# Optimization experiments

Hardware: AMD Instinct MI355X
Metric: run time of the kernel (lower is better)

The kernel has to match this reference:

```python
import jax, jax.numpy as jnp
import numpy as np

N_NODES = 10000
N_EDGES = 160000
F_IN = 2613
D = 256
H = 4
NEG_SLOPE = 0.2
BN_EPS = 1e-5


def _bn(h, g, b):
    # BatchNorm1d in training mode: batch statistics, biased variance
    return (h - h.mean(0)) / jnp.sqrt(h.var(0) + BN_EPS) * g + b


def _gat_conv(h_in, src, dst, n, W, att_src, att_dst, bias):
    # PyG GATConv, concat=True: h_in [n, F] -> [n, H*D]
    h = (h_in @ W).reshape(n, H, D)                      # [n, H, D]
    a_src = jnp.sum(h * att_src, axis=-1)                # [n, H]
    a_dst = jnp.sum(h * att_dst, axis=-1)                # [n, H]
    e = jax.nn.leaky_relu(a_src[src] + a_dst[dst], NEG_SLOPE)  # [E, H]
    # segment softmax over destination nodes (stable)
    m = jax.ops.segment_max(e, dst, num_segments=n)
    e = jnp.exp(e - m[dst])
    denom = jax.ops.segment_sum(e, dst, num_segments=n)
    alpha = e / (denom[dst] + 1e-16)                     # [E, H]
    out = jax.ops.segment_sum(h[src] * alpha[:, :, None], dst, num_segments=n)
    return out.reshape(n, H * D) + bias


def setup_inputs() -> dict:
    key = jax.random.key(0)
    ks = jax.random.split(key, 24)
    s = 0.02
    inp = {
        "x": jax.random.normal(ks[0], (N_NODES, F_IN), jnp.float32),
        "edges": jax.random.randint(ks[1], (2, N_EDGES), 0, N_NODES, jnp.int64),
        # MLP stack
        "W1": jax.random.normal(ks[2], (F_IN, D), jnp.float32) * s,
        "b1": jnp.zeros((D,), jnp.float32),
        "W2": jax.random.normal(ks[3], (D, D), jnp.float32) * s,
        "b2": jnp.zeros((D,), jnp.float32),
        "W3": jax.random.normal(ks[4], (D, D), jnp.float32) * s,
        "b3": jnp.zeros((D,), jnp.float32),
        # BatchNorm affine params
        "g1": jnp.ones((D,), jnp.float32), "be1": jnp.zeros((D,), jnp.float32),
        "g2": jnp.ones((D,), jnp.float32), "be2": jnp.zeros((D,), jnp.float32),
        "g3": jnp.ones((D,), jnp.float32), "be3": jnp.zeros((D,), jnp.float32),
        "g4": jnp.ones((H * D,), jnp.float32), "be4": jnp.zeros((H * D,), jnp.float32),
        "Wg1": jax.random.normal(ks[5], (D, H * D), jnp.float32) * s,
        "as1": jax.random.normal(ks[6], (H, D), jnp.float32) * s,
        "ad1": jax.random.normal(ks[7], (H, D), jnp.float32) * s,
        "bg1": jnp.zeros((H * D,), jnp.float32),
        "Wg2": jax.random.normal(ks[8], (H * D, H * D), jnp.float32) * s,
        "as2": jax.random.normal(ks[9], (H, D), jnp.float32) * s,
        "ad2": jax.random.normal(ks[10], (H, D), jnp.float32) * s,
        "bg2": jnp.zeros((H * D,), jnp.float32),
    }
    return inp


def reference(x, edges, W1, b1, W2, b2, W3, b3,
              g1, be1, g2, be2, g3, be3, g4, be4,
              Wg1, as1, ad1, bg1, Wg2, as2, ad2, bg2):
    n = x.shape[0]
    src, dst = edges[0], edges[1]
    # PyG: remove existing self-loops then add one per node. We reroute
    # accidental self-loops deterministically, then append self-loops.
    dst = jnp.where(src == dst, (dst + 1) % n, dst)
    loops = jnp.arange(n, dtype=src.dtype)
    src = jnp.concatenate([src, loops])
    dst = jnp.concatenate([dst, loops])

    h = jax.nn.elu(_bn(x @ W1 + b1, g1, be1))
    h = jax.nn.elu(_bn(h @ W2 + b2, g2, be2))
    h = jax.nn.elu(_bn(h @ W3 + b3, g3, be3))
    h = _gat_conv(h, src, dst, n, Wg1, as1, ad1, bg1)
    h = jax.nn.elu(_bn(h, g4, be4))
    h = _gat_conv(h, src, dst, n, Wg2, as2, ad2, bg2)
    return h
```

## Files before the change

### kernel.cpp

```cpp
#include <hip/hip_runtime.h>
#include <hip/hip_bf16.h>

typedef __attribute__((ext_vector_type(8))) short short8v;
typedef __attribute__((ext_vector_type(4))) float f32x4;

__device__ inline float b2f(ushort u) {
  union { uint i; float f; } c;
  c.i = (uint)u << 16;
  return c.f;
}
__device__ inline ushort f2b(float f) {
  __hip_bfloat16 h = __float2bfloat16(f);
  return *(ushort*)&h;
}

typedef __attribute__((address_space(1))) const unsigned int guint;
typedef __attribute__((address_space(3))) unsigned int luint;
__device__ __forceinline__ void gload16(const void* g, void* l) {
  __builtin_amdgcn_global_load_lds((guint*)g, (luint*)l, 16, 0, 0);
}

template <bool BN, bool ALIGNED>
__global__ __launch_bounds__(256) void gemm_bn(
    const float* __restrict__ A, const __hip_bfloat16* __restrict__ Bh,
    const __hip_bfloat16* __restrict__ Bl, const float* __restrict__ sc,
    const float* __restrict__ sh, float* __restrict__ P, int M, int N, int K,
    int Kp, int nc, int nr, int nz) {
  __shared__ ushort Ash[128][40];
  __shared__ ushort Asl[128][40];
  __shared__ ushort Bs2[2][128][32];
  __shared__ ushort Bl2[2][128][32];
  const int nwg = gridDim.x;
  const int b = blockIdx.x;
  const int l = (b & 7) * (nwg >> 3) + (b >> 3);
  const int cb = l % nc;
  const int rr = (l / nc) % nr;
  const int z = l / (nc * nr);

  const int tid = threadIdx.x;
  const int lane = tid & 63;
  const int w = tid >> 6, wr = w >> 1, wc = w & 1;
  const int brow = rr * 128, bcol = cb * 128;
  const int l15 = lane & 15, koff = (lane >> 4) * 8;
  const int arow = tid >> 1, aseg = (tid & 1) * 16;
  const int srow = tid >> 2, sseg = (tid & 3) * 8;
  const int nK = (K + 31) >> 5;
  const int ks0 = (nK * z) / nz, ks1 = (nK * (z + 1)) / nz;

  f32x4 acc[4][4] = {};

  const int ar = brow + arow;
  const bool arv = ar < M;
  const float* Arow = A + (long)ar * K;
  const ushort* gBh0 = (const ushort*)Bh + (long)(bcol + srow) * Kp + sseg;
  const ushort* gBh1 = (const ushort*)Bh + (long)(bcol + 64 + srow) * Kp + sseg;
  const ushort* gBl0 = (const ushort*)Bl + (long)(bcol + srow) * Kp + sseg;
  const ushort* gBl1 = (const ushort*)Bl + (long)(bcol + 64 + srow) * Kp + sseg;
  const int lo0 = (w * 64) << 3;
  const int lo1 = (256 + w * 64) << 3;

  float av[16];
  auto loadAv = [&](int ks) {
    const int kb = (ks << 5) + aseg;
    if (arv) {
      if (ALIGNED) {
        const float4* ap = (const float4*)(Arow + kb);
#pragma unroll
        for (int q = 0; q < 4; ++q) {
          float4 f = ap[q];
          av[q * 4 + 0] = f.x;
          av[q * 4 + 1] = f.y;
          av[q * 4 + 2] = f.z;
          av[q * 4 + 3] = f.w;
        }
      } else {
        if (kb + 16 <= K) {
#pragma unroll
          for (int j = 0; j < 16; ++j) av[j] = Arow[kb + j];
        } else {
#pragma unroll
          for (int j = 0; j < 16; ++j) av[j] = (kb + j < K) ? Arow[kb + j] : 0.f;
        }
      }
    } else {
#pragma unroll
      for (int j = 0; j < 16; ++j) av[j] = 0.f;
    }
  };

  if (ks0 < ks1) {
    loadAv(ks0);
    const int k0 = ks0 << 5;
    gload16(gBh0 + k0, &Bs2[0][0][0] + lo0);
    gload16(gBh1 + k0, &Bs2[0][0][0] + lo1);
    gload16(gBl0 + k0, &Bl2[0][0][0] + lo0);
    gload16(gBl1 + k0, &Bl2[0][0][0] + lo1);
  }

  for (int ks = ks0; ks < ks1; ++ks) {
    const int cur = (ks - ks0) & 1;
    const int kbase = (ks << 5) + aseg;
    if (BN && arv) {
#pragma unroll
      for (int q = 0; q < 4; ++q) {
        float4 c4 = *(const float4*)(sc + kbase + q * 4);
        float4 h4 = *(const float4*)(sh + kbase + q * 4);
        float* a4 = &av[q * 4];
        a4[0] = fmaf(a4[0], c4.x, h4.x);
        a4[1] = fmaf(a4[1], c4.y, h4.y);
        a4[2] = fmaf(a4[2], c4.z, h4.z);
        a4[3] = fmaf(a4[3], c4.w, h4.w);
      }
#pragma unroll
      for (int j = 0; j < 16; ++j) {
        float v = av[j];
        av[j] = v > 0.f ? v : (__expf(v) - 1.f);
      }
    }
    short8v ah0, ah1, al0, al1;
#pragma unroll
    for (int j = 0; j < 8; ++j) {
      {
        uint u = __float_as_uint(av[j]);
        ah0[j] = (short)(u >> 16);
        al0[j] = (short)f2b(av[j] - __uint_as_float(u & 0xFFFF0000u));
      }
      {
        uint u = __float_as_uint(av[j + 8]);
        ah1[j] = (short)(u >> 16);
        al1[j] = (short)f2b(av[j + 8] - __uint_as_float(u & 0xFFFF0000u));
      }
    }
    __syncthreads();
    *(short8v*)&Ash[arow][aseg] = ah0;
    *(short8v*)&Ash[arow][aseg + 8] = ah1;
    *(short8v*)&Asl[arow][aseg] = al0;
    *(short8v*)&Asl[arow][aseg + 8] = al1;
    __syncthreads();
    if (ks + 1 < ks1) {
      const int k0n = (ks + 1) << 5;
      const int nxt = cur ^ 1;
      ushort* bh = &Bs2[nxt][0][0];
      ushort* bl = &Bl2[nxt][0][0];
      gload16(gBh0 + k0n, bh + lo0);
      gload16(gBh1 + k0n, bh + lo1);
      gload16(gBl0 + k0n, bl + lo0);
      gload16(gBl1 + k0n, bl + lo1);
      loadAv(ks + 1);
    }
    short8v bfh[4], bfl[4];
#pragma unroll
    for (int nn = 0; nn < 4; ++nn) {
      bfh[nn] = *(const short8v*)&Bs2[cur][wc * 64 + nn * 16 + l15][koff];
      bfl[nn] = *(const short8v*)&Bl2[cur][wc * 64 + nn * 16 + l15][koff];
    }
#pragma unroll
    for (int m = 0; m < 4; ++m) {
      short8v afh = *(const short8v*)&Ash[wr * 64 + m * 16 + l15][koff];
      short8v afl = *(const short8v*)&Asl[wr * 64 + m * 16 + l15][koff];
#pragma unroll
      for (int nn = 0; nn < 4; ++nn) {
        acc[m][nn] = __builtin_amdgcn_mfma_f32_16x16x32_bf16(afh, bfh[nn], acc[m][nn], 0, 0, 0);
        acc[m][nn] = __builtin_amdgcn_mfma_f32_16x16x32_bf16(afh, bfl[nn], acc[m][nn], 0, 0, 0);
        acc[m][nn] = __builtin_amdgcn_mfma_f32_16x16x32_bf16(afl, bfh[nn], acc[m][nn], 0, 0, 0);
      }
    }
  }

  float* outp = P + (long)z * M * N;
#pragma unroll
  for (int m = 0; m < 4; ++m) {
#pragma unroll
    for (int nn = 0; nn < 4; ++nn) {
      int col = bcol + wc * 64 + nn * 16 + l15;
#pragma unroll
      for (int r = 0; r < 4; ++r) {
        int row = brow + wr * 64 + m * 16 + (lane >> 4) * 4 + r;
        if (row < M) outp[(long)row * N + col] = acc[m][nn][r];
      }
    }
  }
}

__global__ __launch_bounds__(256) void gemm_bf16(
    const ushort* __restrict__ A, const __hip_bfloat16* __restrict__ B,
    ushort* __restrict__ C, int M, int N, int K, int nc, int nr) {
  __shared__ ushort A2[2][128][32];
  __shared__ ushort B2[2][128][32];
  const int nwg = gridDim.x;
  const int b = blockIdx.x;
  const int l = (b & 7) * (nwg >> 3) + (b >> 3);
  const int cb = l % nc;
  const int rr = l / nc;

  const int tid = threadIdx.x;
  const int lane = tid & 63;
  const int w = tid >> 6, wr = w >> 1, wc = w & 1;
  const int brow = rr * 128, bcol = cb * 128;
  const int l15 = lane & 15, koff = (lane >> 4) * 8;
  const int srow = tid >> 2, sseg = (tid & 3) * 8;
  const int nK = K >> 5;

  f32x4 acc[4][4] = {};

  const ushort* gA0 = A + (long)(brow + srow) * K + sseg;
  const ushort* gA1 = A + (long)(brow + 64 + srow) * K + sseg;
  const ushort* gB0 = (const ushort*)B + (long)(bcol + srow) * K + sseg;
  const ushort* gB1 = (const ushort*)B + (long)(bcol + 64 + srow) * K + sseg;
  const int lo0 = (w * 64) << 3;
  const int lo1 = (256 + w * 64) << 3;

  gload16(gA0, &A2[0][0][0] + lo0);
  gload16(gA1, &A2[0][0][0] + lo1);
  gload16(gB0, &B2[0][0][0] + lo0);
  gload16(gB1, &B2[0][0][0] + lo1);

  for (int ks = 0; ks < nK; ++ks) {
    const int cur = ks & 1;
    __syncthreads();
    if (ks + 1 < nK) {
      const int k0n = (ks + 1) << 5;
      const int nxt = cur ^ 1;
      gload16(gA0 + k0n, &A2[nxt][0][0] + lo0);
      gload16(gA1 + k0n, &A2[nxt][0][0] + lo1);
      gload16(gB0 + k0n, &B2[nxt][0][0] + lo0);
      gload16(gB1 + k0n, &B2[nxt][0][0] + lo1);
    }
    short8v bf[4];
#pragma unroll
    for (int nn = 0; nn < 4; ++nn)
      bf[nn] = *(const short8v*)&B2[cur][wc * 64 + nn * 16 + l15][koff];
#pragma unroll
    for (int m = 0; m < 4; ++m) {
      short8v af = *(const short8v*)&A2[cur][wr * 64 + m * 16 + l15][koff];
#pragma unroll
      for (int nn = 0; nn < 4; ++nn)
        acc[m][nn] = __builtin_amdgcn_mfma_f32_16x16x32_bf16(af, bf[nn], acc[m][nn], 0, 0, 0);
    }
  }

#pragma unroll
  for (int m = 0; m < 4; ++m) {
#pragma unroll
    for (int nn = 0; nn < 4; ++nn) {
      int col = bcol + wc * 64 + nn * 16 + l15;
#pragma unroll
      for (int r = 0; r < 4; ++r) {
        int row = brow + wr * 64 + m * 16 + (lane >> 4) * 4 + r;
        if (row < M) C[(long)row * N + col] = f2b(acc[m][nn][r]);
      }
    }
  }
}

__global__ __launch_bounds__(256) void bn_elu_b16(
    const float* __restrict__ h, const float* __restrict__ sc,
    const float* __restrict__ sh, ushort* __restrict__ o, long MN, int N) {
  long nq = MN >> 2;
  for (long q = blockIdx.x * 256LL + threadIdx.x; q < nq;
       q += (long)gridDim.x * 256LL) {
    long i = q << 2;
    int col = (int)(i % N);
    float4 v = *(const float4*)(h + i);
    float4 c = *(const float4*)(sc + col);
    float4 s = *(const float4*)(sh + col);
    float a0 = fmaf(v.x, c.x, s.x);
    float a1 = fmaf(v.y, c.y, s.y);
    float a2 = fmaf(v.z, c.z, s.z);
    float a3 = fmaf(v.w, c.w, s.w);
    a0 = a0 > 0.f ? a0 : (__expf(a0) - 1.f);
    a1 = a1 > 0.f ? a1 : (__expf(a1) - 1.f);
    a2 = a2 > 0.f ? a2 : (__expf(a2) - 1.f);
    a3 = a3 > 0.f ? a3 : (__expf(a3) - 1.f);
    ushort4 r;
    r.x = f2b(a0);
    r.y = f2b(a1);
    r.z = f2b(a2);
    r.w = f2b(a3);
    *(ushort4*)(o + i) = r;
  }
}

template <bool BIAS, bool STATS>
__global__ __launch_bounds__(256) void reduce_post(
    const float* __restrict__ P, const float* __restrict__ bias,
    float* __restrict__ C, float* __restrict__ osum, float* __restrict__ osq,
    long MN, int N, int Z) {
  const int col = (int)((blockIdx.x * 256 + threadIdx.x) % N);
  const float bv = BIAS ? bias[col] : 0.f;
  float ps = 0.f, pq = 0.f;
  for (long i = blockIdx.x * 256LL + threadIdx.x; i < MN;
       i += (long)gridDim.x * 256LL) {
    float s = bv;
    for (int zz = 0; zz < Z; ++zz) s += P[(long)zz * MN + i];
    C[i] = s;
    if (STATS) {
      ps += s;
      pq += s * s;
    }
  }
  if (STATS) {
    atomicAdd(&osum[col], ps);
    atomicAdd(&osq[col], pq);
  }
}

__global__ __launch_bounds__(256) void bn_coef(
    const float* __restrict__ ssum, const float* __restrict__ ssq,
    const float* __restrict__ g, const float* __restrict__ be,
    float* __restrict__ sc, float* __restrict__ sh, int N, float invM) {
  int c = blockIdx.x * 256 + threadIdx.x;
  if (c >= N) return;
  float mean = ssum[c] * invM;
  float var = ssq[c] * invM - mean * mean;
  float s = rsqrtf(var + 1e-5f) * g[c];
  sc[c] = s;
  sh[c] = be[c] - mean * s;
}

template <bool LO>
__global__ __launch_bounds__(256) void trans_split(
    const float* __restrict__ W, __hip_bfloat16* __restrict__ Oh,
    __hip_bfloat16* __restrict__ Ol, int K, int N, int Kp) {
  __shared__ float tile[64][65];
  const int k0 = blockIdx.x * 64, n0 = blockIdx.y * 64;
  const int tx = threadIdx.x & 63, ty = threadIdx.x >> 6;
#pragma unroll
  for (int j = 0; j < 16; ++j) {
    int r = ty * 16 + j;
    int k = k0 + r;
    tile[r][tx] = (k < K) ? W[(long)k * N + n0 + tx] : 0.f;
  }
  __syncthreads();
#pragma unroll
  for (int j = 0; j < 16; ++j) {
    int a = ty * 16 + j;
    float v = tile[tx][a];
    long o = (long)(n0 + a) * Kp + k0 + tx;
    if (LO) {
      uint u = __float_as_uint(v);
      ushort hu = (ushort)(u >> 16);
      Oh[o] = *(__hip_bfloat16*)&hu;
      ushort lu = f2b(v - __uint_as_float(u & 0xFFFF0000u));
      Ol[o] = *(__hip_bfloat16*)&lu;
    } else {
      ushort hu = f2b(v);
      Oh[o] = *(__hip_bfloat16*)&hu;
    }
  }
}

__global__ __launch_bounds__(256) void bn_stats(
    const float* __restrict__ h, int M, int N, float* __restrict__ sum,
    float* __restrict__ sumsq) {
  int col = blockIdx.y * 256 + threadIdx.x;
  float s = 0.f, sq = 0.f;
  for (int r = blockIdx.x; r < M; r += gridDim.x) {
    float v = h[(long)r * N + col];
    s += v;
    sq += v * v;
  }
  atomicAdd(&sum[col], s);
  atomicAdd(&sumsq[col], sq);
}

__global__ __launch_bounds__(256) void att_scores_bf16(
    const ushort* __restrict__ hgb, const float* __restrict__ att_s,
    const float* __restrict__ att_d, float* __restrict__ a_src,
    float* __restrict__ a_dst, int n) {
  int node = blockIdx.x;
  int h = threadIdx.x >> 6, lane = threadIdx.x & 63;
  int c = lane * 4;
  ushort4 hv = *(const ushort4*)(hgb + (long)node * 1024 + h * 256 + c);
  float4 as = *(const float4*)(att_s + h * 256 + c);
  float4 ad = *(const float4*)(att_d + h * 256 + c);
  float x0 = b2f(hv.x), x1 = b2f(hv.y), x2 = b2f(hv.z), x3 = b2f(hv.w);
  float ss = x0 * as.x + x1 * as.y + x2 * as.z + x3 * as.w;
  float sd = x0 * ad.x + x1 * ad.y + x2 * ad.z + x3 * ad.w;
#pragma unroll
  for (int off = 32; off; off >>= 1) {
    ss += __shfl_down(ss, off);
    sd += __shfl_down(sd, off);
  }
  if (lane == 0) {
    a_src[node * 4 + h] = ss;
    a_dst[node * 4 + h] = sd;
  }
}

__global__ __launch_bounds__(256) void deg_count(
    const int* __restrict__ srcA, const int* __restrict__ dstA,
    int* __restrict__ deg, int n, int E0, int E) {
  int e = blockIdx.x * blockDim.x + threadIdx.x;
  if (e >= E) return;
  int d;
  if (e < E0) {
    int s = srcA[e];
    d = dstA[e];
    if (s == d) d = (d + 1) % n;
  } else {
    d = e - E0;
  }
  atomicAdd(&deg[d], 1);
}

__global__ __launch_bounds__(256) void scan_rows(
    const int* __restrict__ deg, int* __restrict__ row_start, int n) {
  __shared__ int sums[256];
  int t = threadIdx.x;
  int chunk = (n + 255) / 256;
  int start = t * chunk, end = min(start + chunk, n);
  int s = 0;
  for (int i = start; i < end; ++i) s += deg[i];
  sums[t] = s;
  __syncthreads();
  for (int off = 1; off < 256; off <<= 1) {
    int v = (t >= off) ? sums[t - off] : 0;
    __syncthreads();
    sums[t] += v;
    __syncthreads();
  }
  int run = (t == 0) ? 0 : sums[t - 1];
  for (int i = start; i < end; ++i) {
    row_start[i] = run;
    run += deg[i];
  }
  if (t == 255) row_start[n] = run;
}

__global__ __launch_bounds__(256) void scatter_edges(
    const int* __restrict__ srcA, const int* __restrict__ dstA,
    int* __restrict__ cursor, int* __restrict__ csr_src, int n, int E0, int E) {
  int e = blockIdx.x * blockDim.x + threadIdx.x;
  if (e >= E) return;
  int s, d;
  if (e < E0) {
    s = srcA[e];
    d = dstA[e];
    if (s == d) d = (d + 1) % n;
  } else {
    s = d = e - E0;
  }
  int pos = atomicAdd(&cursor[d], 1);
  csr_src[pos] = s;
}

__global__ __launch_bounds__(256) void aggregate_fused(
    const ushort* __restrict__ hgb, const int* __restrict__ row_start,
    const int* __restrict__ csr_src, const float* __restrict__ a_src,
    const float* __restrict__ a_dst, const float* __restrict__ bias,
    float* __restrict__ out) {
  int d = blockIdx.x;
  int t = threadIdx.x;
  int hh = t >> 6;
  int off = hh * 256 + (t & 63) * 4;
  int p0 = row_start[d], p1 = row_start[d + 1];
  float adv = a_dst[d * 4 + hh];
  float den = 1e-16f;
  float4 acc = {0.f, 0.f, 0.f, 0.f};
  for (int p = p0; p < p1; ++p) {
    int s = csr_src[p];
    float v = a_src[s * 4 + hh] + adv;
    v = v > 0.f ? v : 0.2f * v;
    float ex = __expf(v);
    den += ex;
    ushort4 hv = *(const ushort4*)(hgb + (long)s * 1024 + off);
    acc.x += ex * b2f(hv.x);
    acc.y += ex * b2f(hv.y);
    acc.z += ex * b2f(hv.z);
    acc.w += ex * b2f(hv.w);
  }
  float rden = 1.f / den;
  float4 bv = *(const float4*)(bias + off);
  float4 o;
  o.x = bv.x + acc.x * rden;
  o.y = bv.y + acc.y * rden;
  o.z = bv.z + acc.z * rden;
  o.w = bv.w + acc.w * rden;
  *(float4*)(out + (long)d * 1024 + off) = o;
}

extern "C" void kernel_launch(void* const* d_in, const int* in_sizes, int n_in,
                              void* d_out, int out_size, void* d_ws,
                              size_t ws_size, hipStream_t stream) {
  const float* x = (const float*)d_in[0];
  const int* edges = (const int*)d_in[1];
  const float* W1 = (const float*)d_in[2];
  const float* b1 = (const float*)d_in[3];
  const float* W2 = (const float*)d_in[4];
  const float* b2 = (const float*)d_in[5];
  const float* W3 = (const float*)d_in[6];
  const float* b3 = (const float*)d_in[7];
  const float* g1 = (const float*)d_in[8];
  const float* be1 = (const float*)d_in[9];
  const float* g2 = (const float*)d_in[10];
  const float* be2 = (const float*)d_in[11];
  const float* g3 = (const float*)d_in[12];
  const float* be3 = (const float*)d_in[13];
  const float* g4 = (const float*)d_in[14];
  const float* be4 = (const float*)d_in[15];
  const float* Wg1 = (const float*)d_in[16];
  const float* as1 = (const float*)d_in[17];
  const float* ad1 = (const float*)d_in[18];
  const float* bg1 = (const float*)d_in[19];
  const float* Wg2 = (const float*)d_in[20];
  const float* as2 = (const float*)d_in[21];
  const float* ad2 = (const float*)d_in[22];
  const float* bg2 = (const float*)d_in[23];
  float* out = (float*)d_out;

  const int n = 10000, E0 = 160000, E = 170000;
  const int F = 2613, Fp = 2624, D = 256, HD = 1024;
  const int* srcA = edges;
  const int* dstA = edges + E0;

  uint8_t* p = (uint8_t*)d_ws;
  auto alloc = [&](size_t bytes) -> void* {
    void* r = (void*)p;
    p += (bytes + 255) & ~(size_t)255;
    return r;
  };
  float* h1 = (float*)alloc((size_t)n * D * 4);
  float* h2 = (float*)alloc((size_t)n * D * 4);
  float* h3 = (float*)alloc((size_t)n * D * 4);
  float* agg = (float*)alloc((size_t)n * HD * 4);
  float* pbuf = (float*)alloc((size_t)8 * n * D * 4);
  ushort* hgb = (ushort*)alloc((size_t)n * HD * 2);
  ushort* actb = (ushort*)alloc((size_t)n * HD * 2);
  __hip_bfloat16* W1h = (__hip_bfloat16*)alloc((size_t)D * Fp * 2);
  __hip_bfloat16* W1l = (__hip_bfloat16*)alloc((size_t)D * Fp * 2);
  __hip_bfloat16* W2h = (__hip_bfloat16*)alloc((size_t)D * D * 2);
  __hip_bfloat16* W2l = (__hip_bfloat16*)alloc((size_t)D * D * 2);
  __hip_bfloat16* W3h = (__hip_bfloat16*)alloc((size_t)D * D * 2);
  __hip_bfloat16* W3l = (__hip_bfloat16*)alloc((size_t)D * D * 2);
  __hip_bfloat16* Wg1h = (__hip_bfloat16*)alloc((size_t)HD * D * 2);
  __hip_bfloat16* Wg2h = (__hip_bfloat16*)alloc((size_t)HD * HD * 2);
  float* asrc = (float*)alloc((size_t)n * 4 * 4);
  float* adst = (float*)alloc((size_t)n * 4 * 4);
  float* sc1 = (float*)alloc(D * 4);
  float* sh1 = (float*)alloc(D * 4);
  float* sc2 = (float*)alloc(D * 4);
  float* sh2 = (float*)alloc(D * 4);
  float* sc3 = (float*)alloc(D * 4);
  float* sh3 = (float*)alloc(D * 4);
  float* sc4 = (float*)alloc(HD * 4);
  float* sh4 = (float*)alloc(HD * 4);
  int* row_start = (int*)alloc((size_t)(n + 1) * 4);
  int* cursor = (int*)alloc((size_t)n * 4);
  int* csr_src = (int*)alloc((size_t)E * 4);
  uint8_t* z0 = p;
  float* ssum1 = (float*)alloc(D * 4);
  float* ssq1 = (float*)alloc(D * 4);
  float* ssum2 = (float*)alloc(D * 4);
  float* ssq2 = (float*)alloc(D * 4);
  float* ssum3 = (float*)alloc(D * 4);
  float* ssq3 = (float*)alloc(D * 4);
  float* ssum4 = (float*)alloc(HD * 4);
  float* ssq4 = (float*)alloc(HD * 4);
  int* deg = (int*)alloc((size_t)n * 4);
  size_t zbytes = (size_t)(p - z0);

  dim3 blk(256);
  const int rb = (n + 127) / 128;
  const int eb = (E + 255) / 256;
  const long MN_D = (long)n * D;
  const long MN_HD = (long)n * HD;
  const float invM = 1.f / (float)n;
  const int gL1 = 2 * rb * 8;
  const int gMLP = 2 * rb * 4;
  const int gGAT = 8 * rb;

  hipMemsetAsync(z0, 0, zbytes, stream);

  deg_count<<<eb, blk, 0, stream>>>(srcA, dstA, deg, n, E0, E);
  scan_rows<<<1, blk, 0, stream>>>(deg, row_start, n);
  hipMemcpyAsync(cursor, row_start, n * sizeof(int), hipMemcpyDeviceToDevice, stream);
  scatter_edges<<<eb, blk, 0, stream>>>(srcA, dstA, cursor, csr_src, n, E0, E);

  trans_split<true><<<dim3(Fp / 64, D / 64), blk, 0, stream>>>(W1, W1h, W1l, F, D, Fp);
  trans_split<true><<<dim3(D / 64, D / 64), blk, 0, stream>>>(W2, W2h, W2l, D, D, D);
  trans_split<true><<<dim3(D / 64, D / 64), blk, 0, stream>>>(W3, W3h, W3l, D, D, D);
  trans_split<false><<<dim3(D / 64, HD / 64), blk, 0, stream>>>(Wg1, Wg1h, nullptr, D, HD, D);
  trans_split<false><<<dim3(HD / 64, HD / 64), blk, 0, stream>>>(Wg2, Wg2h, nullptr, HD, HD, HD);

  gemm_bn<false, false><<<gL1, blk, 0, stream>>>(
      x, W1h, W1l, nullptr, nullptr, pbuf, n, D, F, Fp, 2, rb, 8);
  reduce_post<true, true><<<512, blk, 0, stream>>>(pbuf, b1, h1, ssum1, ssq1, MN_D, D, 8);
  bn_coef<<<1, blk, 0, stream>>>(ssum1, ssq1, g1, be1, sc1, sh1, D, invM);

  gemm_bn<true, true><<<gMLP, blk, 0, stream>>>(
      h1, W2h, W2l, sc1, sh1, pbuf, n, D, D, D, 2, rb, 4);
  reduce_post<true, true><<<512, blk, 0, stream>>>(pbuf, b2, h2, ssum2, ssq2, MN_D, D, 4);
  bn_coef<<<1, blk, 0, stream>>>(ssum2, ssq2, g2, be2, sc2, sh2, D, invM);

  gemm_bn<true, true><<<gMLP, blk, 0, stream>>>(
      h2, W3h, W3l, sc2, sh2, pbuf, n, D, D, D, 2, rb, 4);
  reduce_post<true, true><<<512, blk, 0, stream>>>(pbuf, b3, h3, ssum3, ssq3, MN_D, D, 4);
  bn_coef<<<1, blk, 0, stream>>>(ssum3, ssq3, g3, be3, sc3, sh3, D, invM);

  bn_elu_b16<<<1024, blk, 0, stream>>>(h3, sc3, sh3, actb, MN_D, D);
  gemm_bf16<<<gGAT, blk, 0, stream>>>(actb, Wg1h, hgb, n, HD, D, 8, rb);
  att_scores_bf16<<<n, blk, 0, stream>>>(hgb, as1, ad1, asrc, adst, n);
  aggregate_fused<<<n, blk, 0, stream>>>(hgb, row_start, csr_src, asrc, adst, bg1, agg);

  bn_stats<<<dim3(64, HD / 256), blk, 0, stream>>>(agg, n, HD, ssum4, ssq4);
  bn_coef<<<4, blk, 0, stream>>>(ssum4, ssq4, g4, be4, sc4, sh4, HD, invM);
  bn_elu_b16<<<2048, blk, 0, stream>>>(agg, sc4, sh4, actb, MN_HD, HD);

  gemm_bf16<<<gGAT, blk, 0, stream>>>(actb, Wg2h, hgb, n, HD, HD, 8, rb);
  att_scores_bf16<<<n, blk, 0, stream>>>(hgb, as2, ad2, asrc, adst, n);
  aggregate_fused<<<n, blk, 0, stream>>>(hgb, row_start, csr_src, asrc, adst, bg2, out);
}
```

Measured before the change: 560.9 us.

## Convert input to bf16 and use single-precision-bf16 GEMM for first layer

Adds a pre-pass that converts the fp32 input features to zero-padded bf16. The first MLP GEMM then runs through a generalized bf16 GEMM kernel with split-K instead of the three-MFMA hi/lo split emulation. W1 keeps only its high part, and the split-K factor drops from 8 to 4, shrinking the partial buffer. This removes two thirds of the matrix-core work on the largest GEMM, at the cost of an extra conversion pass over the input and reduced numerical accuracy.

```diff
diff --git a/kernel.cpp b/kernel.cpp
--- a/kernel.cpp
+++ b/kernel.cpp
@@ -20,7 +20,105 @@
   __builtin_amdgcn_global_load_lds((guint*)g, (luint*)l, 16, 0, 0);
 }
 
-template <bool BN, bool ALIGNED>
+__global__ __launch_bounds__(256) void cvt_pad(
+    const float* __restrict__ x, ushort* __restrict__ xb, int K, int Kp) {
+  __shared__ ushort row[2624];
+  const int r = blockIdx.x;
+  const float* src = x + (long)r * K;
+  for (int c = threadIdx.x; c < Kp; c += 256)
+    row[c] = (c < K) ? f2b(src[c]) : (ushort)0;
+  __syncthreads();
+  ushort* dst = xb + (long)r * Kp;
+  const int nchunk = Kp >> 3;
+  for (int c = threadIdx.x; c < nchunk; c += 256)
+    *(short8v*)(dst + c * 8) = *(const short8v*)(row + c * 8);
+}
+
+template <bool B16O>
+__global__ __launch_bounds__(256) void gemm_bf16(
+    const ushort* __restrict__ A, const __hip_bfloat16* __restrict__ B,
+    ushort* __restrict__ Cb, float* __restrict__ P, int M, int N, int K,
+    int nc, int nr, int nz) {
+  __shared__ ushort A2[2][128][32];
+  __shared__ ushort B2[2][128][32];
+  const int nwg = gridDim.x;
+  const int b = blockIdx.x;
+  const int l = (b & 7) * (nwg >> 3) + (b >> 3);
+  const int cb = l % nc;
+  const int rr = (l / nc) % nr;
+  const int z = l / (nc * nr);
+
+  const int tid = threadIdx.x;
+  const int lane = tid & 63;
+  const int w = tid >> 6, wr = w >> 1, wc = w & 1;
+  const int brow = rr * 128, bcol = cb * 128;
+  const int l15 = lane & 15, koff = (lane >> 4) * 8;
+  const int srow = tid >> 2, sseg = (tid & 3) * 8;
+  const int nK = K >> 5;
+  const int ks0 = (nK * z) / nz, ks1 = (nK * (z + 1)) / nz;
+
+  f32x4 acc[4][4] = {};
+
+  const ushort* gA0 = A + (long)(brow + srow) * K + sseg;
+  const ushort* gA1 = A + (long)(brow + 64 + srow) * K + sseg;
+  const ushort* gB0 = (const ushort*)B + (long)(bcol + srow) * K + sseg;
+  const ushort* gB1 = (const ushort*)B + (long)(bcol + 64 + srow) * K + sseg;
+  const int lo0 = (w * 64) << 3;
+  const int lo1 = (256 + w * 64) << 3;
+
+  if (ks0 < ks1) {
+    const int k0 = ks0 << 5;
+    gload16(gA0 + k0, &A2[0][0][0] + lo0);
+    gload16(gA1 + k0, &A2[0][0][0] + lo1);
+    gload16(gB0 + k0, &B2[0][0][0] + lo0);
+    gload16(gB1 + k0, &B2[0][0][0] + lo1);
+  }
+
+  for (int ks = ks0; ks < ks1; ++ks) {
+    const int cur = (ks - ks0) & 1;
+    __syncthreads();
+    if (ks + 1 < ks1) {
+      const int k0n = (ks + 1) << 5;
+      const int nxt = cur ^ 1;
+      gload16(gA0 + k0n, &A2[nxt][0][0] + lo0);
+      gload16(gA1 + k0n, &A2[nxt][0][0] + lo1);
+      gload16(gB0 + k0n, &B2[nxt][0][0] + lo0);
+      gload16(gB1 + k0n, &B2[nxt][0][0] + lo1);
+    }
+    short8v bf[4];
+#pragma unroll
+    for (int nn = 0; nn < 4; ++nn)
+      bf[nn] = *(const short8v*)&B2[cur][wc * 64 + nn * 16 + l15][koff];
+#pragma unroll
+    for (int m = 0; m < 4; ++m) {
+      short8v af = *(const short8v*)&A2[cur][wr * 64 + m * 16 + l15][koff];
+#pragma unroll
+      for (int nn = 0; nn < 4; ++nn)
+        acc[m][nn] = __builtin_amdgcn_mfma_f32_16x16x32_bf16(af, bf[nn], acc[m][nn], 0, 0, 0);
+    }
+  }
+
+  float* outp = B16O ? nullptr : P + (long)z * M * N;
+#pragma unroll
+  for (int m = 0; m < 4; ++m) {
+#pragma unroll
+    for (int nn = 0; nn < 4; ++nn) {
+      int col = bcol + wc * 64 + nn * 16 + l15;
+#pragma unroll
+      for (int r = 0; r < 4; ++r) {
+        int row = brow + wr * 64 + m * 16 + (lane >> 4) * 4 + r;
+        if (row < M) {
+          if (B16O)
+            Cb[(long)row * N + col] = f2b(acc[m][nn][r]);
+          else
+            outp[(long)row * N + col] = acc[m][nn][r];
+        }
+      }
+    }
+  }
+}
+
+template <bool BN>
 __global__ __launch_bounds__(256) void gemm_bn(
     const float* __restrict__ A, const __hip_bfloat16* __restrict__ Bh,
     const __hip_bfloat16* __restrict__ Bl, const float* __restrict__ sc,
@@ -63,24 +161,14 @@
   auto loadAv = [&](int ks) {
     const int kb = (ks << 5) + aseg;
     if (arv) {
-      if (ALIGNED) {
-        const float4* ap = (const float4*)(Arow + kb);
-#pragma unroll
-        for (int q = 0; q < 4; ++q) {
-          float4 f = ap[q];
-          av[q * 4 + 0] = f.x;
-          av[q * 4 + 1] = f.y;
-          av[q * 4 + 2] = f.z;
-          av[q * 4 + 3] = f.w;
-        }
-      } else {
-        if (kb + 16 <= K) {
-#pragma unroll
-          for (int j = 0; j < 16; ++j) av[j] = Arow[kb + j];
-        } else {
-#pragma unroll
-          for (int j = 0; j < 16; ++j) av[j] = (kb + j < K) ? Arow[kb + j] : 0.f;
-        }
+      const float4* ap = (const float4*)(Arow + kb);
+#pragma unroll
+      for (int q = 0; q < 4; ++q) {
+        float4 f = ap[q];
+        av[q * 4 + 0] = f.x;
+        av[q * 4 + 1] = f.y;
+        av[q * 4 + 2] = f.z;
+        av[q * 4 + 3] = f.w;
       }
     } else {
 #pragma unroll
@@ -140,12 +228,10 @@
     if (ks + 1 < ks1) {
       const int k0n = (ks + 1) << 5;
       const int nxt = cur ^ 1;
-      ushort* bh = &Bs2[nxt][0][0];
-      ushort* bl = &Bl2[nxt][0][0];
-      gload16(gBh0 + k0n, bh + lo0);
-      gload16(gBh1 + k0n, bh + lo1);
-      gload16(gBl0 + k0n, bl + lo0);
-      gload16(gBl1 + k0n, bl + lo1);
+      gload16(gBh0 + k0n, &Bs2[nxt][0][0] + lo0);
+      gload16(gBh1 + k0n, &Bs2[nxt][0][0] + lo1);
+      gload16(gBl0 + k0n, &Bl2[nxt][0][0] + lo0);
+      gload16(gBl1 + k0n, &Bl2[nxt][0][0] + lo1);
       loadAv(ks + 1);
     }
     short8v bfh[4], bfl[4];
@@ -177,77 +263,6 @@
       for (int r = 0; r < 4; ++r) {
         int row = brow + wr * 64 + m * 16 + (lane >> 4) * 4 + r;
         if (row < M) outp[(long)row * N + col] = acc[m][nn][r];
-      }
-    }
-  }
-}
-
-__global__ __launch_bounds__(256) void gemm_bf16(
-    const ushort* __restrict__ A, const __hip_bfloat16* __restrict__ B,
-    ushort* __restrict__ C, int M, int N, int K, int nc, int nr) {
-  __shared__ ushort A2[2][128][32];
-  __shared__ ushort B2[2][128][32];
-  const int nwg = gridDim.x;
-  const int b = blockIdx.x;
-  const int l = (b & 7) * (nwg >> 3) + (b >> 3);
-  const int cb = l % nc;
-  const int rr = l / nc;
-
-  const int tid = threadIdx.x;
-  const int lane = tid & 63;
-  const int w = tid >> 6, wr = w >> 1, wc = w & 1;
-  const int brow = rr * 128, bcol = cb * 128;
-  const int l15 = lane & 15, koff = (lane >> 4) * 8;
-  const int srow = tid >> 2, sseg = (tid & 3) * 8;
-  const int nK = K >> 5;
-
-  f32x4 acc[4][4] = {};
-
-  const ushort* gA0 = A + (long)(brow + srow) * K + sseg;
-  const ushort* gA1 = A + (long)(brow + 64 + srow) * K + sseg;
-  const ushort* gB0 = (const ushort*)B + (long)(bcol + srow) * K + sseg;
-  const ushort* gB1 = (const ushort*)B + (long)(bcol + 64 + srow) * K + sseg;
-  const int lo0 = (w * 64) << 3;
-  const int lo1 = (256 + w * 64) << 3;
-
-  gload16(gA0, &A2[0][0][0] + lo0);
-  gload16(gA1, &A2[0][0][0] + lo1);
-  gload16(gB0, &B2[0][0][0] + lo0);
-  gload16(gB1, &B2[0][0][0] + lo1);
-
-  for (int ks = 0; ks < nK; ++ks) {
-    const int cur = ks & 1;
-    __syncthreads();
-    if (ks + 1 < nK) {
-      const int k0n = (ks + 1) << 5;
-      const int nxt = cur ^ 1;
-      gload16(gA0 + k0n, &A2[nxt][0][0] + lo0);
-      gload16(gA1 + k0n, &A2[nxt][0][0] + lo1);
-      gload16(gB0 + k0n, &B2[nxt][0][0] + lo0);
-      gload16(gB1 + k0n, &B2[nxt][0][0] + lo1);
-    }
-    short8v bf[4];
-#pragma unroll
-    for (int nn = 0; nn < 4; ++nn)
-      bf[nn] = *(const short8v*)&B2[cur][wc * 64 + nn * 16 + l15][koff];
-#pragma unroll
-    for (int m = 0; m < 4; ++m) {
-      short8v af = *(const short8v*)&A2[cur][wr * 64 + m * 16 + l15][koff];
-#pragma unroll
-      for (int nn = 0; nn < 4; ++nn)
-        acc[m][nn] = __builtin_amdgcn_mfma_f32_16x16x32_bf16(af, bf[nn], acc[m][nn], 0, 0, 0);
-    }
-  }
-
-#pragma unroll
-  for (int m = 0; m < 4; ++m) {
-#pragma unroll
-    for (int nn = 0; nn < 4; ++nn) {
-      int col = bcol + wc * 64 + nn * 16 + l15;
-#pragma unroll
-      for (int r = 0; r < 4; ++r) {
-        int row = brow + wr * 64 + m * 16 + (lane >> 4) * 4 + r;
-        if (row < M) C[(long)row * N + col] = f2b(acc[m][nn][r]);
       }
     }
   }
@@ -520,15 +535,15 @@
     p += (bytes + 255) & ~(size_t)255;
     return r;
   };
+  ushort* xb = (ushort*)alloc((size_t)n * Fp * 2);
   float* h1 = (float*)alloc((size_t)n * D * 4);
   float* h2 = (float*)alloc((size_t)n * D * 4);
   float* h3 = (float*)alloc((size_t)n * D * 4);
   float* agg = (float*)alloc((size_t)n * HD * 4);
-  float* pbuf = (float*)alloc((size_t)8 * n * D * 4);
+  float* pbuf = (float*)alloc((size_t)4 * n * D * 4);
   ushort* hgb = (ushort*)alloc((size_t)n * HD * 2);
   ushort* actb = (ushort*)alloc((size_t)n * HD * 2);
   __hip_bfloat16* W1h = (__hip_bfloat16*)alloc((size_t)D * Fp * 2);
-  __hip_bfloat16* W1l = (__hip_bfloat16*)alloc((size_t)D * Fp * 2);
   __hip_bfloat16* W2h = (__hip_bfloat16*)alloc((size_t)D * D * 2);
   __hip_bfloat16* W2l = (__hip_bfloat16*)alloc((size_t)D * D * 2);
   __hip_bfloat16* W3h = (__hip_bfloat16*)alloc((size_t)D * D * 2);
@@ -566,7 +581,6 @@
   const long MN_D = (long)n * D;
   const long MN_HD = (long)n * HD;
   const float invM = 1.f / (float)n;
-  const int gL1 = 2 * rb * 8;
   const int gMLP = 2 * rb * 4;
   const int gGAT = 8 * rb;
 
@@ -577,29 +591,31 @@
   hipMemcpyAsync(cursor, row_start, n * sizeof(int), hipMemcpyDeviceToDevice, stream);
   scatter_edges<<<eb, blk, 0, stream>>>(srcA, dstA, cursor, csr_src, n, E0, E);
 
-  trans_split<true><<<dim3(Fp / 64, D / 64), blk, 0, stream>>>(W1, W1h, W1l, F, D, Fp);
+  cvt_pad<<<n, blk, 0, stream>>>(x, xb, F, Fp);
+
+  trans_split<false><<<dim3(Fp / 64, D / 64), blk, 0, stream>>>(W1, W1h, nullptr, F, D, Fp);
   trans_split<true><<<dim3(D / 64, D / 64), blk, 0, stream>>>(W2, W2h, W2l, D, D, D);
   trans_split<true><<<dim3(D / 64, D / 64), blk, 0, stream>>>(W3, W3h, W3l, D, D, D);
   trans_split<false><<<dim3(D / 64, HD / 64), blk, 0, stream>>>(Wg1, Wg1h, nullptr, D, HD, D);
   trans_split<false><<<dim3(HD / 64, HD / 64), blk, 0, stream>>>(Wg2, Wg2h, nullptr, HD, HD, HD);
 
-  gemm_bn<false, false><<<gL1, blk, 0, stream>>>(
-      x, W1h, W1l, nullptr, nullptr, pbuf, n, D, F, Fp, 2, rb, 8);
-  reduce_post<true, true><<<512, blk, 0, stream>>>(pbuf, b1, h1, ssum1, ssq1, MN_D, D, 8);
+  gemm_bf16<false><<<gMLP, blk, 0, stream>>>(
+      xb, W1h, nullptr, pbuf, n, D, Fp, 2, rb, 4);
+  reduce_post<true, true><<<512, blk, 0, stream>>>(pbuf, b1, h1, ssum1, ssq1, MN_D, D, 4);
   bn_coef<<<1, blk, 0, stream>>>(ssum1, ssq1, g1, be1, sc1, sh1, D, invM);
 
-  gemm_bn<true, true><<<gMLP, blk, 0, stream>>>(
+  gemm_bn<true><<<gMLP, blk, 0, stream>>>(
       h1, W2h, W2l, sc1, sh1, pbuf, n, D, D, D, 2, rb, 4);
   reduce_post<true, true><<<512, blk, 0, stream>>>(pbuf, b2, h2, ssum2, ssq2, MN_D, D, 4);
   bn_coef<<<1, blk, 0, stream>>>(ssum2, ssq2, g2, be2, sc2, sh2, D, invM);
 
-  gemm_bn<true, true><<<gMLP, blk, 0, stream>>>(
+  gemm_bn<true><<<gMLP, blk, 0, stream>>>(
       h2, W3h, W3l, sc2, sh2, pbuf, n, D, D, D, 2, rb, 4);
   reduce_post<true, true><<<512, blk, 0, stream>>>(pbuf, b3, h3, ssum3, ssq3, MN_D, D, 4);
   bn_coef<<<1, blk, 0, stream>>>(ssum3, ssq3, g3, be3, sc3, sh3, D, invM);
 
   bn_elu_b16<<<1024, blk, 0, stream>>>(h3, sc3, sh3, actb, MN_D, D);
-  gemm_bf16<<<gGAT, blk, 0, stream>>>(actb, Wg1h, hgb, n, HD, D, 8, rb);
+  gemm_bf16<true><<<gGAT, blk, 0, stream>>>(actb, Wg1h, hgb, nullptr, n, HD, D, 8, rb, 1);
   att_scores_bf16<<<n, blk, 0, stream>>>(hgb, as1, ad1, asrc, adst, n);
   aggregate_fused<<<n, blk, 0, stream>>>(hgb, row_start, csr_src, asrc, adst, bg1, agg);
 
@@ -607,7 +623,7 @@
   bn_coef<<<4, blk, 0, stream>>>(ssum4, ssq4, g4, be4, sc4, sh4, HD, invM);
   bn_elu_b16<<<2048, blk, 0, stream>>>(agg, sc4, sh4, actb, MN_HD, HD);
 
-  gemm_bf16<<<gGAT, blk, 0, stream>>>(actb, Wg2h, hgb, n, HD, HD, 8, rb);
+  gemm_bf16<true><<<gGAT, blk, 0, stream>>>(actb, Wg2h, hgb, nullptr, n, HD, HD, 8, rb, 1);
   att_scores_bf16<<<n, blk, 0, stream>>>(hgb, as2, ad2, asrc, adst, n);
   aggregate_fused<<<n, blk, 0, stream>>>(hgb, row_start, csr_src, asrc, adst, bg2, out);
 }
```

After: 544.6 us. -2.9%, faster.

## Drop split-K and bf16x3 for first layer, use 64x64 tiles, remove biases

Applied to the files above, without the earlier changes.

The first MLP GEMM switches from split-bf16 (three MFMAs) with an 8-way split-K and reduction pass to a single-bf16 GEMM. The fp32 input is first converted to a padded bf16 copy. The MLP GEMMs use 64x64 tiles without split-K and write directly to the output, which removes the partial buffer and the reduce_post kernel. BN statistics come from a separate bn_stats pass. Linear biases are dropped because training-mode BN cancels them. The trade-off is lower precision in the large first GEMM, plus an extra conversion pass and an extra stats read.

```diff
diff --git a/kernel.cpp b/kernel.cpp
--- a/kernel.cpp
+++ b/kernel.cpp
@@ -20,146 +20,182 @@
   __builtin_amdgcn_global_load_lds((guint*)g, (luint*)l, 16, 0, 0);
 }
 
-template <bool BN, bool ALIGNED>
-__global__ __launch_bounds__(256) void gemm_bn(
-    const float* __restrict__ A, const __hip_bfloat16* __restrict__ Bh,
-    const __hip_bfloat16* __restrict__ Bl, const float* __restrict__ sc,
-    const float* __restrict__ sh, float* __restrict__ P, int M, int N, int K,
-    int Kp, int nc, int nr, int nz) {
-  __shared__ ushort Ash[128][40];
-  __shared__ ushort Asl[128][40];
-  __shared__ ushort Bs2[2][128][32];
-  __shared__ ushort Bl2[2][128][32];
-  const int nwg = gridDim.x;
-  const int b = blockIdx.x;
-  const int l = (b & 7) * (nwg >> 3) + (b >> 3);
-  const int cb = l % nc;
-  const int rr = (l / nc) % nr;
-  const int z = l / (nc * nr);
+__device__ __forceinline__ int xcd_swz(int b, int nwg) {
+  int q = nwg >> 3, r = nwg & 7;
+  int xcd = b & 7, idx = b >> 3;
+  return (xcd < r ? xcd * (q + 1) : r * (q + 1) + (xcd - r) * q) + idx;
+}
+
+__global__ __launch_bounds__(256) void cvt_pad(
+    const float* __restrict__ x, ushort* __restrict__ xb, int K, int Kp) {
+  __shared__ ushort row[2624];
+  const int r = blockIdx.x;
+  const float* src = x + (long)r * K;
+  for (int c = threadIdx.x; c < Kp; c += 256)
+    row[c] = (c < K) ? f2b(src[c]) : (ushort)0;
+  __syncthreads();
+  ushort* dst = xb + (long)r * Kp;
+  const int nchunk = Kp >> 3;
+  for (int c = threadIdx.x; c < nchunk; c += 256)
+    *(short8v*)(dst + c * 8) = *(const short8v*)(row + c * 8);
+}
+
+__global__ __launch_bounds__(256) void gemm64_b16(
+    const ushort* __restrict__ A, const __hip_bfloat16* __restrict__ B,
+    float* __restrict__ C, int M, int N, int K, int nc) {
+  __shared__ ushort A2[2][64][32];
+  __shared__ ushort B2[2][64][32];
+  const int l = xcd_swz(blockIdx.x, gridDim.x);
+  const int cb = l % nc, rr = l / nc;
 
   const int tid = threadIdx.x;
   const int lane = tid & 63;
   const int w = tid >> 6, wr = w >> 1, wc = w & 1;
-  const int brow = rr * 128, bcol = cb * 128;
+  const int brow = rr * 64, bcol = cb * 64;
   const int l15 = lane & 15, koff = (lane >> 4) * 8;
-  const int arow = tid >> 1, aseg = (tid & 1) * 16;
   const int srow = tid >> 2, sseg = (tid & 3) * 8;
-  const int nK = (K + 31) >> 5;
-  const int ks0 = (nK * z) / nz, ks1 = (nK * (z + 1)) / nz;
-
-  f32x4 acc[4][4] = {};
+  const int nK = K >> 5;
+
+  f32x4 acc[2][2] = {};
+
+  const ushort* gA = A + (long)(brow + srow) * K + sseg;
+  const ushort* gB = (const ushort*)B + (long)(bcol + srow) * K + sseg;
+  const int lo = (w * 16 * 32);
+
+  gload16(gA, &A2[0][0][0] + lo);
+  gload16(gB, &B2[0][0][0] + lo);
+
+  for (int ks = 0; ks < nK; ++ks) {
+    const int cur = ks & 1;
+    __syncthreads();
+    if (ks + 1 < nK) {
+      const int k0n = (ks + 1) << 5;
+      const int nxt = cur ^ 1;
+      gload16(gA + k0n, &A2[nxt][0][0] + lo);
+      gload16(gB + k0n, &B2[nxt][0][0] + lo);
+    }
+    short8v bf[2];
+#pragma unroll
+    for (int nn = 0; nn < 2; ++nn)
+      bf[nn] = *(const short8v*)&B2[cur][wc * 32 + nn * 16 + l15][koff];
+#pragma unroll
+    for (int m = 0; m < 2; ++m) {
+      short8v af = *(const short8v*)&A2[cur][wr * 32 + m * 16 + l15][koff];
+#pragma unroll
+      for (int nn = 0; nn < 2; ++nn)
+        acc[m][nn] = __builtin_amdgcn_mfma_f32_16x16x32_bf16(af, bf[nn], acc[m][nn], 0, 0, 0);
+    }
+  }
+
+#pragma unroll
+  for (int m = 0; m < 2; ++m) {
+#pragma unroll
+    for (int nn = 0; nn < 2; ++nn) {
+      int col = bcol + wc * 32 + nn * 16 + l15;
+#pragma unroll
+      for (int r = 0; r < 4; ++r) {
+        int row = brow + wr * 32 + m * 16 + (lane >> 4) * 4 + r;
+        if (row < M) C[(long)row * N + col] = acc[m][nn][r];
+      }
+    }
+  }
+}
+
+__global__ __launch_bounds__(256) void gemm64_bn(
+    const float* __restrict__ A, const __hip_bfloat16* __restrict__ Bh,
+    const __hip_bfloat16* __restrict__ Bl, const float* __restrict__ sc,
+    const float* __restrict__ sh, float* __restrict__ C, int M, int N, int K,
+    int nc) {
+  __shared__ ushort Ash[64][32];
+  __shared__ ushort Asl[64][32];
+  __shared__ ushort Bs2[2][64][32];
+  __shared__ ushort Bl2[2][64][32];
+  const int l = xcd_swz(blockIdx.x, gridDim.x);
+  const int cb = l % nc, rr = l / nc;
+
+  const int tid = threadIdx.x;
+  const int lane = tid & 63;
+  const int w = tid >> 6, wr = w >> 1, wc = w & 1;
+  const int brow = rr * 64, bcol = cb * 64;
+  const int l15 = lane & 15, koff = (lane >> 4) * 8;
+  const int arow = tid >> 2, aseg = (tid & 3) * 8;
+  const int nK = K >> 5;
+
+  f32x4 acc[2][2] = {};
 
   const int ar = brow + arow;
   const bool arv = ar < M;
   const float* Arow = A + (long)ar * K;
-  const ushort* gBh0 = (const ushort*)Bh + (long)(bcol + srow) * Kp + sseg;
-  const ushort* gBh1 = (const ushort*)Bh + (long)(bcol + 64 + srow) * Kp + sseg;
-  const ushort* gBl0 = (const ushort*)Bl + (long)(bcol + srow) * Kp + sseg;
-  const ushort* gBl1 = (const ushort*)Bl + (long)(bcol + 64 + srow) * Kp + sseg;
-  const int lo0 = (w * 64) << 3;
-  const int lo1 = (256 + w * 64) << 3;
-
-  float av[16];
+  const ushort* gBh = (const ushort*)Bh + (long)(bcol + arow) * K + aseg;
+  const ushort* gBl = (const ushort*)Bl + (long)(bcol + arow) * K + aseg;
+  const int lo = (w * 16 * 32);
+
+  float av[8];
   auto loadAv = [&](int ks) {
     const int kb = (ks << 5) + aseg;
     if (arv) {
-      if (ALIGNED) {
-        const float4* ap = (const float4*)(Arow + kb);
-#pragma unroll
-        for (int q = 0; q < 4; ++q) {
-          float4 f = ap[q];
-          av[q * 4 + 0] = f.x;
-          av[q * 4 + 1] = f.y;
-          av[q * 4 + 2] = f.z;
-          av[q * 4 + 3] = f.w;
-        }
-      } else {
-        if (kb + 16 <= K) {
-#pragma unroll
-          for (int j = 0; j < 16; ++j) av[j] = Arow[kb + j];
-        } else {
-#pragma unroll
-          for (int j = 0; j < 16; ++j) av[j] = (kb + j < K) ? Arow[kb + j] : 0.f;
-        }
-      }
+      const float4* ap = (const float4*)(Arow + kb);
+      float4 f0 = ap[0], f1 = ap[1];
+      av[0] = f0.x; av[1] = f0.y; av[2] = f0.z; av[3] = f0.w;
+      av[4] = f1.x; av[5] = f1.y; av[6] = f1.z; av[7] = f1.w;
     } else {
 #pragma unroll
-      for (int j = 0; j < 16; ++j) av[j] = 0.f;
+      for (int j = 0; j < 8; ++j) av[j] = 0.f;
     }
   };
 
-  if (ks0 < ks1) {
-    loadAv(ks0);
-    const int k0 = ks0 << 5;
-    gload16(gBh0 + k0, &Bs2[0][0][0] + lo0);
-    gload16(gBh1 + k0, &Bs2[0][0][0] + lo1);
-    gload16(gBl0 + k0, &Bl2[0][0][0] + lo0);
-    gload16(gBl1 + k0, &Bl2[0][0][0] + lo1);
-  }
-
-  for (int ks = ks0; ks < ks1; ++ks) {
-    const int cur = (ks - ks0) & 1;
+  loadAv(0);
+  gload16(gBh, &Bs2[0][0][0] + lo);
+  gload16(gBl, &Bl2[0][0][0] + lo);
+
+  for (int ks = 0; ks < nK; ++ks) {
+    const int cur = ks & 1;
     const int kbase = (ks << 5) + aseg;
-    if (BN && arv) {
-#pragma unroll
-      for (int q = 0; q < 4; ++q) {
-        float4 c4 = *(const float4*)(sc + kbase + q * 4);
-        float4 h4 = *(const float4*)(sh + kbase + q * 4);
-        float* a4 = &av[q * 4];
-        a4[0] = fmaf(a4[0], c4.x, h4.x);
-        a4[1] = fmaf(a4[1], c4.y, h4.y);
-        a4[2] = fmaf(a4[2], c4.z, h4.z);
-        a4[3] = fmaf(a4[3], c4.w, h4.w);
-      }
-#pragma unroll
-      for (int j = 0; j < 16; ++j) {
+    if (arv) {
+      float4 c0 = *(const float4*)(sc + kbase);
+      float4 c1 = *(const float4*)(sc + kbase + 4);
+      float4 s0 = *(const float4*)(sh + kbase);
+      float4 s1 = *(const float4*)(sh + kbase + 4);
+      av[0] = fmaf(av[0], c0.x, s0.x); av[1] = fmaf(av[1], c0.y, s0.y);
+      av[2] = fmaf(av[2], c0.z, s0.z); av[3] = fmaf(av[3], c0.w, s0.w);
+      av[4] = fmaf(av[4], c1.x, s1.x); av[5] = fmaf(av[5], c1.y, s1.y);
+      av[6] = fmaf(av[6], c1.z, s1.z); av[7] = fmaf(av[7], c1.w, s1.w);
+#pragma unroll
+      for (int j = 0; j < 8; ++j) {
         float v = av[j];
         av[j] = v > 0.f ? v : (__expf(v) - 1.f);
       }
     }
-    short8v ah0, ah1, al0, al1;
+    short8v ah, al;
 #pragma unroll
     for (int j = 0; j < 8; ++j) {
-      {
-        uint u = __float_as_uint(av[j]);
-        ah0[j] = (short)(u >> 16);
-        al0[j] = (short)f2b(av[j] - __uint_as_float(u & 0xFFFF0000u));
-      }
-      {
-        uint u = __float_as_uint(av[j + 8]);
-        ah1[j] = (short)(u >> 16);
-        al1[j] = (short)f2b(av[j + 8] - __uint_as_float(u & 0xFFFF0000u));
-      }
+      uint u = __float_as_uint(av[j]);
+      ah[j] = (short)(u >> 16);
+      al[j] = (short)f2b(av[j] - __uint_as_float(u & 0xFFFF0000u));
     }
     __syncthreads();
-    *(short8v*)&Ash[arow][aseg] = ah0;
-    *(short8v*)&Ash[arow][aseg + 8] = ah1;
-    *(short8v*)&Asl[arow][aseg] = al0;
-    *(short8v*)&Asl[arow][aseg + 8] = al1;
+    *(short8v*)&Ash[arow][aseg] = ah;
+    *(short8v*)&Asl[arow][aseg] = al;
     __syncthreads();
-    if (ks + 1 < ks1) {
+    if (ks + 1 < nK) {
       const int k0n = (ks + 1) << 5;
       const int nxt = cur ^ 1;
-      ushort* bh = &Bs2[nxt][0][0];
-      ushort* bl = &Bl2[nxt][0][0];
-      gload16(gBh0 + k0n, bh + lo0);
-      gload16(gBh1 + k0n, bh + lo1);
-      gload16(gBl0 + k0n, bl + lo0);
-      gload16(gBl1 + k0n, bl + lo1);
+      gload16(gBh + k0n, &Bs2[nxt][0][0] + lo);
+      gload16(gBl + k0n, &Bl2[nxt][0][0] + lo);
       loadAv(ks + 1);
     }
-    short8v bfh[4], bfl[4];
-#pragma unroll
-    for (int nn = 0; nn < 4; ++nn) {
-      bfh[nn] = *(const short8v*)&Bs2[cur][wc * 64 + nn * 16 + l15][koff];
-      bfl[nn] = *(const short8v*)&Bl2[cur][wc * 64 + nn * 16 + l15][koff];
-    }
-#pragma unroll
-    for (int m = 0; m < 4; ++m) {
-      short8v afh = *(const short8v*)&Ash[wr * 64 + m * 16 + l15][koff];
-      short8v afl = *(const short8v*)&Asl[wr * 64 + m * 16 + l15][koff];
-#pragma unroll
-      for (int nn = 0; nn < 4; ++nn) {
+    short8v bfh[2], bfl[2];
+#pragma unroll
+    for (int nn = 0; nn < 2; ++nn) {
+      bfh[nn] = *(const short8v*)&Bs2[cur][wc * 32 + nn * 16 + l15][koff];
+      bfl[nn] = *(const short8v*)&Bl2[cur][wc * 32 + nn * 16 + l15][koff];
+    }
+#pragma unroll
+    for (int m = 0; m < 2; ++m) {
+      short8v afh = *(const short8v*)&Ash[wr * 32 + m * 16 + l15][koff];
+      short8v afl = *(const short8v*)&Asl[wr * 32 + m * 16 + l15][koff];
+#pragma unroll
+      for (int nn = 0; nn < 2; ++nn) {
         acc[m][nn] = __builtin_amdgcn_mfma_f32_16x16x32_bf16(afh, bfh[nn], acc[m][nn], 0, 0, 0);
         acc[m][nn] = __builtin_amdgcn_mfma_f32_16x16x32_bf16(afh, bfl[nn], acc[m][nn], 0, 0, 0);
         acc[m][nn] = __builtin_amdgcn_mfma_f32_16x16x32_bf16(afl, bfh[nn], acc[m][nn], 0, 0, 0);
@@ -167,16 +203,15 @@
     }
   }
 
-  float* outp = P + (long)z * M * N;
-#pragma unroll
-  for (int m = 0; m < 4; ++m) {
-#pragma unroll
-    for (int nn = 0; nn < 4; ++nn) {
-      int col = bcol + wc * 64 + nn * 16 + l15;
+#pragma unroll
+  for (int m = 0; m < 2; ++m) {
+#pragma unroll
+    for (int nn = 0; nn < 2; ++nn) {
+      int col = bcol + wc * 32 + nn * 16 + l15;
 #pragma unroll
       for (int r = 0; r < 4; ++r) {
-        int row = brow + wr * 64 + m * 16 + (lane >> 4) * 4 + r;
-        if (row < M) outp[(long)row * N + col] = acc[m][nn][r];
+        int row = brow + wr * 32 + m * 16 + (lane >> 4) * 4 + r;
+        if (row < M) C[(long)row * N + col] = acc[m][nn][r];
       }
     }
   }
@@ -281,30 +316,6 @@
   }
 }
 
-template <bool BIAS, bool STATS>
-__global__ __launch_bounds__(256) void reduce_post(
-    const float* __restrict__ P, const float* __restrict__ bias,
-    float* __restrict__ C, float* __restrict__ osum, float* __restrict__ osq,
-    long MN, int N, int Z) {
-  const int col = (int)((blockIdx.x * 256 + threadIdx.x) % N);
-  const float bv = BIAS ? bias[col] : 0.f;
-  float ps = 0.f, pq = 0.f;
-  for (long i = blockIdx.x * 256LL + threadIdx.x; i < MN;
-       i += (long)gridDim.x * 256LL) {
-    float s = bv;
-    for (int zz = 0; zz < Z; ++zz) s += P[(long)zz * MN + i];
-    C[i] = s;
-    if (STATS) {
-      ps += s;
-      pq += s * s;
-    }
-  }
-  if (STATS) {
-    atomicAdd(&osum[col], ps);
-    atomicAdd(&osq[col], pq);
-  }
-}
-
 __global__ __launch_bounds__(256) void bn_coef(
     const float* __restrict__ ssum, const float* __restrict__ ssq,
     const float* __restrict__ g, const float* __restrict__ be,
@@ -486,11 +497,8 @@
   const float* x = (const float*)d_in[0];
   const int* edges = (const int*)d_in[1];
   const float* W1 = (const float*)d_in[2];
-  const float* b1 = (const float*)d_in[3];
   const float* W2 = (const float*)d_in[4];
-  const float* b2 = (const float*)d_in[5];
   const float* W3 = (const float*)d_in[6];
-  const float* b3 = (const float*)d_in[7];
   const float* g1 = (const float*)d_in[8];
   const float* be1 = (const float*)d_in[9];
   const float* g2 = (const float*)d_in[10];
@@ -520,15 +528,14 @@
     p += (bytes + 255) & ~(size_t)255;
     return r;
   };
+  ushort* xb = (ushort*)alloc((size_t)n * Fp * 2);
   float* h1 = (float*)alloc((size_t)n * D * 4);
   float* h2 = (float*)alloc((size_t)n * D * 4);
   float* h3 = (float*)alloc((size_t)n * D * 4);
   float* agg = (float*)alloc((size_t)n * HD * 4);
-  float* pbuf = (float*)alloc((size_t)8 * n * D * 4);
   ushort* hgb = (ushort*)alloc((size_t)n * HD * 2);
   ushort* actb = (ushort*)alloc((size_t)n * HD * 2);
   __hip_bfloat16* W1h = (__hip_bfloat16*)alloc((size_t)D * Fp * 2);
-  __hip_bfloat16* W1l = (__hip_bfloat16*)alloc((size_t)D * Fp * 2);
   __hip_bfloat16* W2h = (__hip_bfloat16*)alloc((size_t)D * D * 2);
   __hip_bfloat16* W2l = (__hip_bfloat16*)alloc((size_t)D * D * 2);
   __hip_bfloat16* W3h = (__hip_bfloat16*)alloc((size_t)D * D * 2);
@@ -562,12 +569,12 @@
 
   dim3 blk(256);
   const int rb = (n + 127) / 128;
+  const int rb64 = (n + 63) / 64;
   const int eb = (E + 255) / 256;
   const long MN_D = (long)n * D;
   const long MN_HD = (long)n * HD;
   const float invM = 1.f / (float)n;
-  const int gL1 = 2 * rb * 8;
-  const int gMLP = 2 * rb * 4;
+  const int gMLP = 4 * rb64;
   const int gGAT = 8 * rb;
 
   hipMemsetAsync(z0, 0, zbytes, stream);
@@ -577,25 +584,24 @@
   hipMemcpyAsync(cursor, row_start, n * sizeof(int), hipMemcpyDeviceToDevice, stream);
   scatter_edges<<<eb, blk, 0, stream>>>(srcA, dstA, cursor, csr_src, n, E0, E);
 
-  trans_split<true><<<dim3(Fp / 64, D / 64), blk, 0, stream>>>(W1, W1h, W1l, F, D, Fp);
+  cvt_pad<<<n, blk, 0, stream>>>(x, xb, F, Fp);
+
+  trans_split<false><<<dim3(Fp / 64, D / 64), blk, 0, stream>>>(W1, W1h, nullptr, F, D, Fp);
   trans_split<true><<<dim3(D / 64, D / 64), blk, 0, stream>>>(W2, W2h, W2l, D, D, D);
   trans_split<true><<<dim3(D / 64, D / 64), blk, 0, stream>>>(W3, W3h, W3l, D, D, D);
   trans_split<false><<<dim3(D / 64, HD / 64), blk, 0, stream>>>(Wg1, Wg1h, nullptr, D, HD, D);
   trans_split<false><<<dim3(HD / 64, HD / 64), blk, 0, stream>>>(Wg2, Wg2h, nullptr, HD, HD, HD);
 
-  gemm_bn<false, false><<<gL1, blk, 0, stream>>>(
-      x, W1h, W1l, nullptr, nullptr, pbuf, n, D, F, Fp, 2, rb, 8);
-  reduce_post<true, true><<<512, blk, 0, stream>>>(pbuf, b1, h1, ssum1, ssq1, MN_D, D, 8);
+  gemm64_b16<<<gMLP, blk, 0, stream>>>(xb, W1h, h1, n, D, Fp, 4);
+  bn_stats<<<dim3(64, 1), blk, 0, stream>>>(h1, n, D, ssum1, ssq1);
   bn_coef<<<1, blk, 0, stream>>>(ssum1, ssq1, g1, be1, sc1, sh1, D, invM);
 
-  gemm_bn<true, true><<<gMLP, blk, 0, stream>>>(
-      h1, W2h, W2l, sc1, sh1, pbuf, n, D, D, D, 2, rb, 4);
-  reduce_post<true, true><<<512, blk, 0, stream>>>(pbuf, b2, h2, ssum2, ssq2, MN_D, D, 4);
+  gemm64_bn<<<gMLP, blk, 0, stream>>>(h1, W2h, W2l, sc1, sh1, h2, n, D, D, 4);
+  bn_stats<<<dim3(64, 1), blk, 0, stream>>>(h2, n, D, ssum2, ssq2);
   bn_coef<<<1, blk, 0, stream>>>(ssum2, ssq2, g2, be2, sc2, sh2, D, invM);
 
-  gemm_bn<true, true><<<gMLP, blk, 0, stream>>>(
-      h2, W3h, W3l, sc2, sh2, pbuf, n, D, D, D, 2, rb, 4);
-  reduce_post<true, true><<<512, blk, 0, stream>>>(pbuf, b3, h3, ssum3, ssq3, MN_D, D, 4);
+  gemm64_bn<<<gMLP, blk, 0, stream>>>(h2, W3h, W3l, sc2, sh2, h3, n, D, D, 4);
+  bn_stats<<<dim3(64, 1), blk, 0, stream>>>(h3, n, D, ssum3, ssq3);
   bn_coef<<<1, blk, 0, stream>>>(ssum3, ssq3, g3, be3, sc3, sh3, D, invM);
 
   bn_elu_b16<<<1024, blk, 0, stream>>>(h3, sc3, sh3, actb, MN_D, D);
```

Result: no change. 561.0 us (+0.0%).
